# Kernel optimization log

Measured on AMD Instinct MI355X. Metric: run time of the kernel, lower is better.

The kernel has to match this reference:

```python
import jax, jax.numpy as jnp
import numpy as np

N_NODES = 10000
AVG_DEG = 16
N_EDGES = N_NODES * AVG_DEG
NODE_DIM, EDGE_DIM, LIN_DIM, HID, OUT, LAYERS = 9, 3, 32, 300, 2, 5


def _init(key, shape, fan_in):
    return jax.random.normal(key, shape, jnp.float32) * (1.0 / np.sqrt(fan_in))


def setup_inputs() -> dict:
    key = jax.random.key(0)
    ks = jax.random.split(key, 18)
    inp = {
        "x": jax.random.normal(ks[0], (N_NODES, NODE_DIM), jnp.float32),
        "edge_index": jax.random.randint(ks[1], (2, N_EDGES), 0, N_NODES, jnp.int32),
        "edge_attr": jax.random.normal(ks[2], (N_EDGES, EDGE_DIM), jnp.float32),
        "batch": jnp.zeros((N_NODES,), jnp.int32),
        # nn.Linear params (stored as [in, out] so fwd is x @ W + b)
        "node_w": _init(ks[3], (NODE_DIM, LIN_DIM), NODE_DIM),
        "node_b": jnp.zeros((LIN_DIM,), jnp.float32),
        "edge_w": _init(ks[4], (EDGE_DIM, LIN_DIM), EDGE_DIM),
        "edge_b": jnp.zeros((LIN_DIM,), jnp.float32),
        # GCNConv: lin (no bias) + separate additive bias (PyG convention)
        "gcn0_w": _init(ks[5], (LIN_DIM, HID), LIN_DIM),
        "gcn0_b": jnp.zeros((HID,), jnp.float32),
        "gcn_w": _init(ks[6], (LAYERS - 1, HID, HID), HID),
        "gcn_b": jnp.zeros((LAYERS - 1, HID), jnp.float32),
        "lin1_w": _init(ks[7], (HID, LIN_DIM), HID),
        "lin1_b": jnp.zeros((LIN_DIM,), jnp.float32),
        "lin2_w": _init(ks[8], (LIN_DIM, OUT), LIN_DIM),
        "lin2_b": jnp.zeros((OUT,), jnp.float32),
    }
    return inp


def reference(x, edge_index, edge_attr, batch,
              node_w, node_b, edge_w, edge_b,
              gcn0_w, gcn0_b, gcn_w, gcn_b,
              lin1_w, lin1_b, lin2_w, lin2_b):
    row, col = edge_index[0], edge_index[1]

    e = edge_attr @ edge_w + edge_b  # [E, LIN_DIM] edge embeddings

    # Faithful to the original bug: node embeddings get edge attrs scatter-added,
    # then the result is discarded by `attr = edge_attr`. Kept for fidelity (dead).
    node_h = x @ node_w + node_b
    node_h = node_h.at[row].add(e)  # unused downstream

    # GCN stack runs over the E-row edge-embedding matrix -> effective node count = E
    h = e
    n = h.shape[0]  # == N_EDGES

    # symmetric gcn_norm with self-loops (edge_weight = 1), computed once
    deg = jax.ops.segment_sum(jnp.ones((edge_index.shape[1],), h.dtype), col,
                              num_segments=n) + 1.0
    dinv = jax.lax.rsqrt(deg)
    norm = dinv[row] * dinv[col]  # per-edge normalization
    self_norm = (dinv * dinv)[:, None]  # self-loop term

    def gcn(h, w, b):
        hw = h @ w  # dense transform
        agg = jax.ops.segment_sum(hw[row] * norm[:, None], col, num_segments=n)
        return agg + self_norm * hw + b

    h = jax.nn.relu(gcn(h, gcn0_w, gcn0_b))

    def step(h, wb):
        w, b = wb
        return jax.nn.relu(gcn(h, w, b)), None

    h, _ = jax.lax.scan(step, h, (gcn_w, gcn_b))

    g = jnp.mean(h, axis=0, keepdims=True)  # [1, HID] graph readout
    g = jax.nn.relu(g @ lin1_w + lin1_b)
    pred = g @ lin2_w + lin2_b  # [1, OUT]; forward returns pre-softmax logits
    return pred
```

## Files before the change

### kernel.cpp

```cpp
#include <hip/hip_runtime.h>
#include <hip/hip_bf16.h>

#define N_NODES 10000
#define N_EDGES 160000
#define HID 300
#define HIDP 304
#define NPARTB (N_EDGES - N_NODES)
#define RB 64
#define KS 328

typedef __attribute__((ext_vector_type(8))) short short8;
typedef __attribute__((ext_vector_type(4))) float f32x4;

#define MFMA_B16(a, b, c) __builtin_amdgcn_mfma_f32_16x16x32_bf16(a, b, c, 0, 0, 0)

__device__ __forceinline__ short bf16r(float x) {
    unsigned u = __float_as_uint(x);
    return (short)((u + 0x7fffu + ((u >> 16) & 1u)) >> 16);
}

__device__ __forceinline__ float b2f(unsigned short u) {
    return __uint_as_float(((unsigned)u) << 16);
}

__device__ __forceinline__ void split1(float x, short& hi, short& lo) {
    short h = bf16r(x);
    float hf = __uint_as_float(((unsigned)(unsigned short)h) << 16);
    hi = h;
    lo = bf16r(x - hf);
}


__global__ void k_count(const int* __restrict__ col, int* __restrict__ cnt) {
    int e = blockIdx.x * 256 + threadIdx.x;
    if (e < N_EDGES) atomicAdd(&cnt[col[e]], 1);
}

__global__ void k_scan(const int* __restrict__ cnt, int* __restrict__ col_start,
                       int* __restrict__ cursor, float* __restrict__ dinv,
                       float* __restrict__ selfnorm) {
    __shared__ int wsum[4];
    int t = threadIdx.x;
    int lane = t & 63, w = t >> 6;
    int carry = 0;
    for (int base = 0; base < N_NODES; base += 256) {
        int i = base + t;
        int v = (i < N_NODES) ? cnt[i] : 0;
        int s = v;
#pragma unroll
        for (int d = 1; d < 64; d <<= 1) {
            int n = __shfl_up(s, d, 64);
            if (lane >= d) s += n;
        }
        if (lane == 63) wsum[w] = s;
        __syncthreads();
        int woff = 0;
#pragma unroll
        for (int k = 0; k < 4; ++k)
            if (k < w) woff += wsum[k];
        int total = wsum[0] + wsum[1] + wsum[2] + wsum[3];
        if (i < N_NODES) {
            int excl = carry + woff + s - v;
            col_start[i] = excl;
            cursor[i] = excl;
            float dd = (float)v + 1.0f;
            dinv[i] = rsqrtf(dd);
            selfnorm[i] = 1.0f / dd;
        }
        carry += total;
        __syncthreads();
    }
    if (t == 0) col_start[N_NODES] = carry;
}

__global__ void k_fill(const int* __restrict__ row, const int* __restrict__ col,
                       int* __restrict__ cursor, const float* __restrict__ dinv,
                       int2* __restrict__ edge_pack) {
    int e = blockIdx.x * 256 + threadIdx.x;
    if (e < N_EDGES) {
        int c = col[e], r = row[e];
        int p = atomicAdd(&cursor[c], 1);
        edge_pack[p] = make_int2(r, __float_as_int(dinv[r] * dinv[c]));
    }
}

__global__ void k_wt(const float* __restrict__ g0w, const float* __restrict__ gw,
                     short* __restrict__ wt0, short* __restrict__ wtl) {
    int idx = blockIdx.x * 256 + threadIdx.x;
    if (idx < 1216) {
        int n16 = idx & 15, q = (idx >> 4) & 3, nt = idx >> 6;
        int n = nt * 16 + n16;
        short* hd = wt0 + (size_t)(nt * 8 + q) * 128 + n16 * 8;
        short* ld = wt0 + (size_t)(nt * 8 + 4 + q) * 128 + n16 * 8;
#pragma unroll
        for (int j = 0; j < 8; ++j) {
            int k = q * 8 + j;
            float f = (n < HID) ? g0w[k * HID + n] : 0.0f;
            short hi, lo;
            split1(f, hi, lo);
            hd[j] = hi;
            ld[j] = lo;
        }
    } else if (idx < 1216 + 48640) {
        int i = idx - 1216;
        int n16 = i & 15; i >>= 4;
        int q = i & 3; i >>= 2;
        int nt = i % 19; i /= 19;
        int chunk = i % 10;
        int l = i / 10;
        int n = nt * 16 + n16;
        int cnt_idx = chunk * 19 + nt;
        short* base = wtl + (size_t)l * 194560;
        short* hd = base + (size_t)(cnt_idx * 8 + q) * 128 + n16 * 8;
        short* ld = base + (size_t)(cnt_idx * 8 + 4 + q) * 128 + n16 * 8;
#pragma unroll
        for (int j = 0; j < 8; ++j) {
            int k = chunk * 32 + q * 8 + j;
            float f = (k < HID && n < HID) ? gw[((size_t)l * HID + k) * HID + n] : 0.0f;
            short hi, lo;
            split1(f, hi, lo);
            hd[j] = hi;
            ld[j] = lo;
        }
    }
}


template <int NTC>
__device__ __forceinline__ void kloop(const short* __restrict__ wp, int nch,
                                      const short* Hh,
                                      int nt0, int quad, int l16,
                                      f32x4 (&acc)[4][3]) {
#pragma unroll
    for (int mt = 0; mt < 4; ++mt)
#pragma unroll
        for (int i = 0; i < NTC; ++i)
#pragma unroll
            for (int r = 0; r < 4; ++r) acc[mt][i][r] = 0.0f;
#pragma unroll 1
    for (int c = 0; c < nch; ++c) {
        short8 ah[4];
#pragma unroll
        for (int mt = 0; mt < 4; ++mt)
            ah[mt] = *(const short8*)&Hh[(mt * 16 + l16) * KS + c * 32 + quad * 8];
        const short* cb = wp + (size_t)(c * 19 + nt0) * 1024 + quad * 128 + l16 * 8;
        short8 bb[NTC];
#pragma unroll
        for (int i = 0; i < NTC; ++i) bb[i] = *(const short8*)(cb + (size_t)i * 1024);
#pragma unroll
        for (int mt = 0; mt < 4; ++mt)
#pragma unroll
            for (int i = 0; i < NTC; ++i)
                acc[mt][i] = MFMA_B16(ah[mt], bb[i], acc[mt][i]);
#pragma unroll
        for (int i = 0; i < NTC; ++i) bb[i] = *(const short8*)(cb + (size_t)i * 1024 + 512);
#pragma unroll
        for (int mt = 0; mt < 4; ++mt)
#pragma unroll
            for (int i = 0; i < NTC; ++i)
                acc[mt][i] = MFMA_B16(ah[mt], bb[i], acc[mt][i]);
    }
}

template <int NTC>
__device__ __forceinline__ void gcn_epilogue(const float* __restrict__ bias,
                                             int nt0, int quad, int l16,
                                             f32x4 (&acc)[4][3], short* Hh) {
#pragma unroll
    for (int i = 0; i < NTC; ++i) {
        int c = (nt0 + i) * 16 + l16;
        float b = (c < HID) ? bias[c] : 0.0f;
#pragma unroll
        for (int mt = 0; mt < 4; ++mt)
#pragma unroll
            for (int r = 0; r < 4; ++r) {
                float v = fmaxf(acc[mt][i][r] + b, 0.0f);
                Hh[(mt * 16 + quad * 4 + r) * KS + c] = bf16r(v);
            }
    }
}

template <int NTC>
__device__ __forceinline__ void gcn_final(const float* __restrict__ bias,
                                          int nt0, int quad, int l16,
                                          int valid, int slot,
                                          f32x4 (&acc)[4][3],
                                          float* __restrict__ g_part) {
#pragma unroll
    for (int i = 0; i < NTC; ++i) {
        int c = (nt0 + i) * 16 + l16;
        float b = (c < HID) ? bias[c] : 0.0f;
        float s = 0.0f;
#pragma unroll
        for (int mt = 0; mt < 4; ++mt)
#pragma unroll
            for (int r = 0; r < 4; ++r) {
                int rr = mt * 16 + quad * 4 + r;
                float v = fmaxf(acc[mt][i][r] + b, 0.0f);
                if (rr < valid) s += v;
            }
        s += __shfl_xor(s, 16, 64);
        s += __shfl_xor(s, 32, 64);
        if (quad == 0 && c < HID)
            atomicAdd(&g_part[slot * HIDP + c], s);
    }
}

__global__ __launch_bounds__(512, 4) void k_partB_mfma(
    const float* __restrict__ edge_attr,
    const float* __restrict__ edge_w,
    const float* __restrict__ edge_b,
    const short* __restrict__ wt0,
    const short* __restrict__ wtl,
    const float* __restrict__ b0,
    const float* __restrict__ gb,
    float* __restrict__ g_part) {
    __shared__ short Hh[RB * KS];
    int t = threadIdx.x;
    int lane = t & 63, w = t >> 6;
    int l16 = lane & 15, quad = lane >> 4;
    int base = N_NODES + blockIdx.x * RB;
    int nt0 = (w < 3) ? w * 3 : 9 + (w - 3) * 2;
    int valid = N_EDGES - base;

    {
        int r = t >> 3, c4 = (t & 7) * 4;
        int gr = base + r;
        float a0 = 0.f, a1 = 0.f, a2 = 0.f;
        if (gr < N_EDGES) {
            const float* ar = edge_attr + (size_t)gr * 3;
            a0 = ar[0]; a1 = ar[1]; a2 = ar[2];
        }
#pragma unroll
        for (int j = 0; j < 4; ++j) {
            int cc = c4 + j;
            float v = 0.0f;
            if (gr < N_EDGES) {
                v = edge_b[cc];
                v = fmaf(a0, edge_w[cc], v);
                v = fmaf(a1, edge_w[32 + cc], v);
                v = fmaf(a2, edge_w[64 + cc], v);
            }
            Hh[r * KS + cc] = bf16r(v);
        }
    }
    for (int i = t; i < RB * 24; i += 512) {
        int r = i / 24, k = 304 + i % 24;
        Hh[r * KS + k] = 0;
    }
    __syncthreads();

    f32x4 acc[4][3];
    if (w < 3) kloop<3>(wt0, 1, Hh, nt0, quad, l16, acc);
    else       kloop<2>(wt0, 1, Hh, nt0, quad, l16, acc);
    __syncthreads();
    if (w < 3) gcn_epilogue<3>(b0, nt0, quad, l16, acc, Hh);
    else       gcn_epilogue<2>(b0, nt0, quad, l16, acc, Hh);
    __syncthreads();

    for (int l = 0; l < 4; ++l) {
        const short* wp = wtl + (size_t)l * 194560;
        const float* bias = gb + l * HID;
        if (w < 3) kloop<3>(wp, 10, Hh, nt0, quad, l16, acc);
        else       kloop<2>(wp, 10, Hh, nt0, quad, l16, acc);
        __syncthreads();
        if (l < 3) {
            if (w < 3) gcn_epilogue<3>(bias, nt0, quad, l16, acc, Hh);
            else       gcn_epilogue<2>(bias, nt0, quad, l16, acc, Hh);
            __syncthreads();
        } else {
            int slot = (blockIdx.x + w) & 63;
            if (w < 3) gcn_final<3>(bias, nt0, quad, l16, valid, slot, acc, g_part);
            else       gcn_final<2>(bias, nt0, quad, l16, valid, slot, acc, g_part);
        }
    }
}

template <int NTC>
__device__ __forceinline__ void gemm_out(int base, int nt0, int quad, int l16,
                                         f32x4 (&acc)[4][3],
                                         unsigned short* __restrict__ HW) {
#pragma unroll
    for (int i = 0; i < NTC; ++i) {
        int c = (nt0 + i) * 16 + l16;
#pragma unroll
        for (int mt = 0; mt < 4; ++mt)
#pragma unroll
            for (int r = 0; r < 4; ++r) {
                int gm = base + mt * 16 + quad * 4 + r;
                if (gm < N_NODES)
                    HW[(size_t)gm * HIDP + c] = (unsigned short)bf16r(acc[mt][i][r]);
            }
    }
}

template <bool L0>
__global__ __launch_bounds__(512, 4) void k_gemmA(
    const unsigned short* __restrict__ A,
    const float* __restrict__ edge_attr,
    const float* __restrict__ edge_w,
    const float* __restrict__ edge_b,
    const short* __restrict__ wt,
    unsigned short* __restrict__ HW) {
    __shared__ short Hh[RB * KS];
    int t = threadIdx.x;
    int lane = t & 63, w = t >> 6;
    int l16 = lane & 15, quad = lane >> 4;
    int base = blockIdx.x * RB;
    int nt0 = (w < 3) ? w * 3 : 9 + (w - 3) * 2;

    if (L0) {
        int r = t >> 3, c4 = (t & 7) * 4;
        int gr = base + r;
        float a0 = 0.f, a1 = 0.f, a2 = 0.f;
        if (gr < N_NODES) {
            const float* ar = edge_attr + (size_t)gr * 3;
            a0 = ar[0]; a1 = ar[1]; a2 = ar[2];
        }
#pragma unroll
        for (int j = 0; j < 4; ++j) {
            int cc = c4 + j;
            float v = 0.0f;
            if (gr < N_NODES) {
                v = edge_b[cc];
                v = fmaf(a0, edge_w[cc], v);
                v = fmaf(a1, edge_w[32 + cc], v);
                v = fmaf(a2, edge_w[64 + cc], v);
            }
            Hh[r * KS + cc] = bf16r(v);
        }
    } else {
        for (int idx = t; idx < RB * 76; idx += 512) {
            int r = idx / 76, c4 = (idx % 76) * 4;
            int gr = base + r;
            ushort4 v = make_ushort4(0, 0, 0, 0);
            if (gr < N_NODES) v = *(const ushort4*)(A + (size_t)gr * HIDP + c4);
            short* d = &Hh[r * KS + c4];
            d[0] = (short)v.x; d[1] = (short)v.y; d[2] = (short)v.z; d[3] = (short)v.w;
        }
        for (int i = t; i < RB * 24; i += 512) {
            int r = i / 24, k = 304 + i % 24;
            Hh[r * KS + k] = 0;
        }
    }
    __syncthreads();

    f32x4 acc[4][3];
    if (L0) {
        if (w < 3) kloop<3>(wt, 1, Hh, nt0, quad, l16, acc);
        else       kloop<2>(wt, 1, Hh, nt0, quad, l16, acc);
    } else {
        if (w < 3) kloop<3>(wt, 10, Hh, nt0, quad, l16, acc);
        else       kloop<2>(wt, 10, Hh, nt0, quad, l16, acc);
    }
    if (w < 3) gemm_out<3>(base, nt0, quad, l16, acc, HW);
    else       gemm_out<2>(base, nt0, quad, l16, acc, HW);
}

__global__ __launch_bounds__(256) void k_aggA(
    const unsigned short* __restrict__ hw, const int* __restrict__ col_start,
    const int2* __restrict__ edge_pack, const float* __restrict__ selfnorm,
    const float* __restrict__ bias, unsigned short* __restrict__ out) {
    int wid = (blockIdx.x * 256 + threadIdx.x) >> 6;
    int lane = threadIdx.x & 63;
    int c = __builtin_amdgcn_readfirstlane(wid);
    if (c >= N_NODES) return;
    int beg = col_start[c], end = col_start[c + 1];
    float v[5] = {0.0f, 0.0f, 0.0f, 0.0f, 0.0f};
    int i = beg;
    for (; i + 4 <= end; i += 4) {
        int2 e0 = edge_pack[i], e1 = edge_pack[i + 1];
        int2 e2 = edge_pack[i + 2], e3 = edge_pack[i + 3];
        const unsigned short* h0 = hw + (size_t)e0.x * HIDP;
        const unsigned short* h1 = hw + (size_t)e1.x * HIDP;
        const unsigned short* h2 = hw + (size_t)e2.x * HIDP;
        const unsigned short* h3 = hw + (size_t)e3.x * HIDP;
        float n0 = __int_as_float(e0.y), n1 = __int_as_float(e1.y);
        float n2 = __int_as_float(e2.y), n3 = __int_as_float(e3.y);
#pragma unroll
        for (int j = 0; j < 5; ++j) {
            int col = lane + 64 * j;
            if (col < HIDP) {
                float s = v[j];
                s = fmaf(n0, b2f(h0[col]), s);
                s = fmaf(n1, b2f(h1[col]), s);
                s = fmaf(n2, b2f(h2[col]), s);
                s = fmaf(n3, b2f(h3[col]), s);
                v[j] = s;
            }
        }
    }
    for (; i < end; ++i) {
        int2 e0 = edge_pack[i];
        const unsigned short* h0 = hw + (size_t)e0.x * HIDP;
        float n0 = __int_as_float(e0.y);
#pragma unroll
        for (int j = 0; j < 5; ++j) {
            int col = lane + 64 * j;
            if (col < HIDP) v[j] = fmaf(n0, b2f(h0[col]), v[j]);
        }
    }
    float sn = selfnorm[c];
    const unsigned short* sp = hw + (size_t)c * HIDP;
#pragma unroll
    for (int j = 0; j < 5; ++j) {
        int col = lane + 64 * j;
        if (col < HIDP) {
            float h = v[j] + sn * b2f(sp[col]) + ((col < HID) ? bias[col] : 0.0f);
            out[(size_t)c * HIDP + col] = (unsigned short)bf16r(fmaxf(h, 0.0f));
        }
    }
}

__global__ void k_colsum(const unsigned short* __restrict__ h,
                         const float* __restrict__ g_part,
                         float* __restrict__ g_sum) {
    int b = blockIdx.x, t = threadIdx.x;
    if (b < 157) {
        int r0 = b * 64;
        float s0 = 0.0f, s1 = 0.0f;
        for (int r = 0; r < 64; ++r) {
            int gr = r0 + r;
            if (gr < N_NODES) {
                s0 += b2f(h[(size_t)gr * HIDP + t]);
                if (t < HIDP - 256) s1 += b2f(h[(size_t)gr * HIDP + 256 + t]);
            }
        }
        if (t < HID) atomicAdd(&g_sum[t], s0);
        if (t < HIDP - 256 && 256 + t < HID) atomicAdd(&g_sum[256 + t], s1);
    } else {
        int cc = (b - 157) * 256 + t;
        if (cc < HID) {
            float s = 0.0f;
            for (int g = 0; g < 64; ++g) s += g_part[g * HIDP + cc];
            atomicAdd(&g_sum[cc], s);
        }
    }
}

__global__ void k_head(const float* __restrict__ g_sum,
                       const float* __restrict__ lin1_w, const float* __restrict__ lin1_b,
                       const float* __restrict__ lin2_w, const float* __restrict__ lin2_b,
                       float* __restrict__ out) {
    __shared__ float g2[32];
    int t = threadIdx.x;
    const float inv = 1.0f / (float)N_EDGES;
    if (t < 32) {
        float a = lin1_b[t];
        for (int d = 0; d < HID; ++d) a = fmaf(g_sum[d] * inv, lin1_w[d * 32 + t], a);
        g2[t] = fmaxf(a, 0.0f);
    }
    __syncthreads();
    if (t < 2) {
        float p = lin2_b[t];
        for (int j = 0; j < 32; ++j) p = fmaf(g2[j], lin2_w[j * 2 + t], p);
        out[t] = p;
    }
}


extern "C" void kernel_launch(void* const* d_in, const int* in_sizes, int n_in,
                              void* d_out, int out_size, void* d_ws, size_t ws_size,
                              hipStream_t stream) {
    (void)in_sizes; (void)n_in; (void)out_size; (void)ws_size;
    const int* edge_index = (const int*)d_in[1];
    const float* edge_attr = (const float*)d_in[2];
    const float* edge_w = (const float*)d_in[6];
    const float* edge_b = (const float*)d_in[7];
    const float* gcn0_w = (const float*)d_in[8];
    const float* gcn0_b = (const float*)d_in[9];
    const float* gcn_w = (const float*)d_in[10];
    const float* gcn_b = (const float*)d_in[11];
    const float* lin1_w = (const float*)d_in[12];
    const float* lin1_b = (const float*)d_in[13];
    const float* lin2_w = (const float*)d_in[14];
    const float* lin2_b = (const float*)d_in[15];

    char* ws = (char*)d_ws;
    size_t off = 0;
    auto alloc = [&](size_t bytes) {
        void* p = ws + off;
        off = (off + bytes + 255) & ~(size_t)255;
        return p;
    };
    unsigned short* hA = (unsigned short*)alloc((size_t)N_NODES * HIDP * 2);
    unsigned short* hB = (unsigned short*)alloc((size_t)N_NODES * HIDP * 2);
    unsigned short* hw = (unsigned short*)alloc((size_t)N_NODES * HIDP * 2);
    int2* edge_pack = (int2*)alloc((size_t)N_EDGES * 8);
    int* cnt = (int*)alloc((size_t)N_NODES * 4);
    int* col_start = (int*)alloc((size_t)(N_NODES + 1) * 4);
    int* cursor = (int*)alloc((size_t)N_NODES * 4);
    float* dinv = (float*)alloc((size_t)N_NODES * 4);
    float* selfnorm = (float*)alloc((size_t)N_NODES * 4);
    float* g_sum = (float*)alloc((size_t)HIDP * 4);
    short* wt0 = (short*)alloc((size_t)38912);
    short* wtl = (short*)alloc((size_t)4 * 389120);
    float* g_part = (float*)alloc((size_t)64 * HIDP * 4);

    const int* row = edge_index;
    const int* col = edge_index + N_EDGES;

    hipMemsetAsync(cnt, 0, N_NODES * 4, stream);
    hipMemsetAsync(g_sum, 0, HIDP * 4, stream);
    hipMemsetAsync(g_part, 0, 64 * HIDP * 4, stream);

    k_wt<<<(1216 + 48640 + 255) / 256, 256, 0, stream>>>(gcn0_w, gcn_w, wt0, wtl);
    k_count<<<(N_EDGES + 255) / 256, 256, 0, stream>>>(col, cnt);
    k_scan<<<1, 256, 0, stream>>>(cnt, col_start, cursor, dinv, selfnorm);
    k_fill<<<(N_EDGES + 255) / 256, 256, 0, stream>>>(row, col, cursor, dinv, edge_pack);

    k_partB_mfma<<<(NPARTB + RB - 1) / RB, 512, 0, stream>>>(
        edge_attr, edge_w, edge_b, wt0, wtl, gcn0_b, gcn_b, g_part);

    const int gA_blocks = (N_NODES + RB - 1) / RB;
    const int aggA_blocks = (N_NODES + 3) / 4;
    k_gemmA<true><<<gA_blocks, 512, 0, stream>>>(nullptr, edge_attr, edge_w, edge_b, wt0, hw);
    k_aggA<<<aggA_blocks, 256, 0, stream>>>(hw, col_start, edge_pack, selfnorm, gcn0_b, hA);
    unsigned short* curr = hA;
    unsigned short* next = hB;
    for (int l = 1; l < 5; ++l) {
        k_gemmA<false><<<gA_blocks, 512, 0, stream>>>(curr, edge_attr, edge_w, edge_b,
                                                      wtl + (size_t)(l - 1) * 194560, hw);
        k_aggA<<<aggA_blocks, 256, 0, stream>>>(hw, col_start, edge_pack, selfnorm,
                                                gcn_b + (l - 1) * HID, next);
        unsigned short* tmp = curr; curr = next; next = tmp;
    }
    k_colsum<<<159, 256, 0, stream>>>(curr, g_part, g_sum);
    k_head<<<1, 64, 0, stream>>>(g_sum, lin1_w, lin1_b, lin2_w, lin2_b, (float*)d_out);
}
```

Measured before the change: 545.6 us.

## Fuse GCN stages into a mega-kernel and fused aggregate+GEMM kernels

The separate part-B, layer-0 GEMM and CSR-fill kernels become one heterogeneous mega-kernel dispatched by block index, and the count step is folded into weight preparation. Each layer's aggregation is fused with the next layer's GEMM, and the final aggregation is fused with the column-sum readout. Row tile size drops from 64 to 48 so 150000 part-B rows divide evenly, which removes bounds checks and allows higher occupancy. The aim is fewer launches and fewer intermediate HBM round trips, at the cost of less MFMA reuse per block and possibly imbalanced work across block types.

```diff
diff --git a/kernel.cpp b/kernel.cpp
--- a/kernel.cpp
+++ b/kernel.cpp
@@ -6,8 +6,12 @@
 #define HID 300
 #define HIDP 304
 #define NPARTB (N_EDGES - N_NODES)
-#define RB 64
+#define RB 48
 #define KS 328
+#define PARTB_BLOCKS 3125
+#define GEMMA_BLOCKS 209
+#define FILL_BLOCKS 313
+#define MEGA_BLOCKS (PARTB_BLOCKS + GEMMA_BLOCKS + FILL_BLOCKS)
 
 typedef __attribute__((ext_vector_type(8))) short short8;
 typedef __attribute__((ext_vector_type(4))) float f32x4;
@@ -30,63 +34,11 @@
     lo = bf16r(x - hf);
 }
 
-
-__global__ void k_count(const int* __restrict__ col, int* __restrict__ cnt) {
-    int e = blockIdx.x * 256 + threadIdx.x;
-    if (e < N_EDGES) atomicAdd(&cnt[col[e]], 1);
-}
-
-__global__ void k_scan(const int* __restrict__ cnt, int* __restrict__ col_start,
-                       int* __restrict__ cursor, float* __restrict__ dinv,
-                       float* __restrict__ selfnorm) {
-    __shared__ int wsum[4];
-    int t = threadIdx.x;
-    int lane = t & 63, w = t >> 6;
-    int carry = 0;
-    for (int base = 0; base < N_NODES; base += 256) {
-        int i = base + t;
-        int v = (i < N_NODES) ? cnt[i] : 0;
-        int s = v;
-#pragma unroll
-        for (int d = 1; d < 64; d <<= 1) {
-            int n = __shfl_up(s, d, 64);
-            if (lane >= d) s += n;
-        }
-        if (lane == 63) wsum[w] = s;
-        __syncthreads();
-        int woff = 0;
-#pragma unroll
-        for (int k = 0; k < 4; ++k)
-            if (k < w) woff += wsum[k];
-        int total = wsum[0] + wsum[1] + wsum[2] + wsum[3];
-        if (i < N_NODES) {
-            int excl = carry + woff + s - v;
-            col_start[i] = excl;
-            cursor[i] = excl;
-            float dd = (float)v + 1.0f;
-            dinv[i] = rsqrtf(dd);
-            selfnorm[i] = 1.0f / dd;
-        }
-        carry += total;
-        __syncthreads();
-    }
-    if (t == 0) col_start[N_NODES] = carry;
-}
-
-__global__ void k_fill(const int* __restrict__ row, const int* __restrict__ col,
-                       int* __restrict__ cursor, const float* __restrict__ dinv,
-                       int2* __restrict__ edge_pack) {
-    int e = blockIdx.x * 256 + threadIdx.x;
-    if (e < N_EDGES) {
-        int c = col[e], r = row[e];
-        int p = atomicAdd(&cursor[c], 1);
-        edge_pack[p] = make_int2(r, __float_as_int(dinv[r] * dinv[c]));
-    }
-}
-
-__global__ void k_wt(const float* __restrict__ g0w, const float* __restrict__ gw,
-                     short* __restrict__ wt0, short* __restrict__ wtl) {
+__global__ void k_prep(const float* __restrict__ g0w, const float* __restrict__ gw,
+                       short* __restrict__ wt0, short* __restrict__ wtl,
+                       const int* __restrict__ col, int* __restrict__ cnt) {
     int idx = blockIdx.x * 256 + threadIdx.x;
+    if (idx < N_EDGES) atomicAdd(&cnt[col[idx]], 1);
     if (idx < 1216) {
         int n16 = idx & 15, q = (idx >> 4) & 3, nt = idx >> 6;
         int n = nt * 16 + n16;
@@ -125,37 +77,73 @@
     }
 }
 
+__global__ void k_scan(const int* __restrict__ cnt, int* __restrict__ col_start,
+                       int* __restrict__ cursor, float* __restrict__ dinv,
+                       float* __restrict__ selfnorm) {
+    __shared__ int wsum[4];
+    int t = threadIdx.x;
+    int lane = t & 63, w = t >> 6;
+    int carry = 0;
+    for (int base = 0; base < N_NODES; base += 256) {
+        int i = base + t;
+        int v = (i < N_NODES) ? cnt[i] : 0;
+        int s = v;
+#pragma unroll
+        for (int d = 1; d < 64; d <<= 1) {
+            int n = __shfl_up(s, d, 64);
+            if (lane >= d) s += n;
+        }
+        if (lane == 63) wsum[w] = s;
+        __syncthreads();
+        int woff = 0;
+#pragma unroll
+        for (int k = 0; k < 4; ++k)
+            if (k < w) woff += wsum[k];
+        int total = wsum[0] + wsum[1] + wsum[2] + wsum[3];
+        if (i < N_NODES) {
+            int excl = carry + woff + s - v;
+            col_start[i] = excl;
+            cursor[i] = excl;
+            float dd = (float)v + 1.0f;
+            dinv[i] = rsqrtf(dd);
+            selfnorm[i] = 1.0f / dd;
+        }
+        carry += total;
+        __syncthreads();
+    }
+    if (t == 0) col_start[N_NODES] = carry;
+}
 
 template <int NTC>
 __device__ __forceinline__ void kloop(const short* __restrict__ wp, int nch,
                                       const short* Hh,
                                       int nt0, int quad, int l16,
-                                      f32x4 (&acc)[4][3]) {
-#pragma unroll
-    for (int mt = 0; mt < 4; ++mt)
+                                      f32x4 (&acc)[3][3]) {
+#pragma unroll
+    for (int mt = 0; mt < 3; ++mt)
 #pragma unroll
         for (int i = 0; i < NTC; ++i)
 #pragma unroll
             for (int r = 0; r < 4; ++r) acc[mt][i][r] = 0.0f;
 #pragma unroll 1
     for (int c = 0; c < nch; ++c) {
-        short8 ah[4];
-#pragma unroll
-        for (int mt = 0; mt < 4; ++mt)
+        const short* cb = wp + (size_t)(c * 19 + nt0) * 1024 + quad * 128 + l16 * 8;
+        short8 ah[3];
+#pragma unroll
+        for (int mt = 0; mt < 3; ++mt)
             ah[mt] = *(const short8*)&Hh[(mt * 16 + l16) * KS + c * 32 + quad * 8];
-        const short* cb = wp + (size_t)(c * 19 + nt0) * 1024 + quad * 128 + l16 * 8;
         short8 bb[NTC];
 #pragma unroll
         for (int i = 0; i < NTC; ++i) bb[i] = *(const short8*)(cb + (size_t)i * 1024);
 #pragma unroll
-        for (int mt = 0; mt < 4; ++mt)
+        for (int mt = 0; mt < 3; ++mt)
 #pragma unroll
             for (int i = 0; i < NTC; ++i)
                 acc[mt][i] = MFMA_B16(ah[mt], bb[i], acc[mt][i]);
 #pragma unroll
         for (int i = 0; i < NTC; ++i) bb[i] = *(const short8*)(cb + (size_t)i * 1024 + 512);
 #pragma unroll
-        for (int mt = 0; mt < 4; ++mt)
+        for (int mt = 0; mt < 3; ++mt)
 #pragma unroll
             for (int i = 0; i < NTC; ++i)
                 acc[mt][i] = MFMA_B16(ah[mt], bb[i], acc[mt][i]);
@@ -165,13 +153,13 @@
 template <int NTC>
 __device__ __forceinline__ void gcn_epilogue(const float* __restrict__ bias,
                                              int nt0, int quad, int l16,
-                                             f32x4 (&acc)[4][3], short* Hh) {
+                                             f32x4 (&acc)[3][3], short* Hh) {
 #pragma unroll
     for (int i = 0; i < NTC; ++i) {
         int c = (nt0 + i) * 16 + l16;
         float b = (c < HID) ? bias[c] : 0.0f;
 #pragma unroll
-        for (int mt = 0; mt < 4; ++mt)
+        for (int mt = 0; mt < 3; ++mt)
 #pragma unroll
             for (int r = 0; r < 4; ++r) {
                 float v = fmaxf(acc[mt][i][r] + b, 0.0f);
@@ -182,9 +170,8 @@
 
 template <int NTC>
 __device__ __forceinline__ void gcn_final(const float* __restrict__ bias,
-                                          int nt0, int quad, int l16,
-                                          int valid, int slot,
-                                          f32x4 (&acc)[4][3],
+                                          int nt0, int quad, int l16, int slot,
+                                          f32x4 (&acc)[3][3],
                                           float* __restrict__ g_part) {
 #pragma unroll
     for (int i = 0; i < NTC; ++i) {
@@ -192,13 +179,9 @@
         float b = (c < HID) ? bias[c] : 0.0f;
         float s = 0.0f;
 #pragma unroll
-        for (int mt = 0; mt < 4; ++mt)
-#pragma unroll
-            for (int r = 0; r < 4; ++r) {
-                int rr = mt * 16 + quad * 4 + r;
-                float v = fmaxf(acc[mt][i][r] + b, 0.0f);
-                if (rr < valid) s += v;
-            }
+        for (int mt = 0; mt < 3; ++mt)
+#pragma unroll
+            for (int r = 0; r < 4; ++r) s += fmaxf(acc[mt][i][r] + b, 0.0f);
         s += __shfl_xor(s, 16, 64);
         s += __shfl_xor(s, 32, 64);
         if (quad == 0 && c < HID)
@@ -206,102 +189,185 @@
     }
 }
 
-__global__ __launch_bounds__(512, 4) void k_partB_mfma(
+template <int NTC>
+__device__ __forceinline__ void gemm_out(int base, int nt0, int quad, int l16,
+                                         f32x4 (&acc)[3][3],
+                                         unsigned short* __restrict__ HW) {
+#pragma unroll
+    for (int i = 0; i < NTC; ++i) {
+        int c = (nt0 + i) * 16 + l16;
+#pragma unroll
+        for (int mt = 0; mt < 3; ++mt)
+#pragma unroll
+            for (int r = 0; r < 4; ++r) {
+                int gm = base + mt * 16 + quad * 4 + r;
+                if (gm < N_NODES)
+                    HW[(size_t)gm * HIDP + c] = (unsigned short)bf16r(acc[mt][i][r]);
+            }
+    }
+}
+
+__global__ __launch_bounds__(512, 6) void k_mega(
     const float* __restrict__ edge_attr,
     const float* __restrict__ edge_w,
     const float* __restrict__ edge_b,
     const short* __restrict__ wt0,
     const short* __restrict__ wtl,
-    const float* __restrict__ b0,
-    const float* __restrict__ gb,
-    float* __restrict__ g_part) {
+    const float* __restrict__ gcn0_b,
+    const float* __restrict__ gcn_b,
+    float* __restrict__ g_part,
+    unsigned short* __restrict__ hw0,
+    const int* __restrict__ row,
+    const int* __restrict__ col,
+    int* __restrict__ cursor,
+    const float* __restrict__ dinv,
+    int2* __restrict__ edge_pack) {
     __shared__ short Hh[RB * KS];
-    int t = threadIdx.x;
+    int bid = blockIdx.x, t = threadIdx.x;
     int lane = t & 63, w = t >> 6;
     int l16 = lane & 15, quad = lane >> 4;
-    int base = N_NODES + blockIdx.x * RB;
     int nt0 = (w < 3) ? w * 3 : 9 + (w - 3) * 2;
-    int valid = N_EDGES - base;
-
-    {
-        int r = t >> 3, c4 = (t & 7) * 4;
-        int gr = base + r;
-        float a0 = 0.f, a1 = 0.f, a2 = 0.f;
-        if (gr < N_EDGES) {
-            const float* ar = edge_attr + (size_t)gr * 3;
-            a0 = ar[0]; a1 = ar[1]; a2 = ar[2];
-        }
-#pragma unroll
-        for (int j = 0; j < 4; ++j) {
-            int cc = c4 + j;
-            float v = 0.0f;
-            if (gr < N_EDGES) {
-                v = edge_b[cc];
+
+    if (bid < PARTB_BLOCKS) {
+        int base = N_NODES + bid * RB;
+        if (t < 384) {
+            int r = t >> 3, c4 = (t & 7) * 4;
+            const float* ar = edge_attr + (size_t)(base + r) * 3;
+            float a0 = ar[0], a1 = ar[1], a2 = ar[2];
+#pragma unroll
+            for (int j = 0; j < 4; ++j) {
+                int cc = c4 + j;
+                float v = edge_b[cc];
                 v = fmaf(a0, edge_w[cc], v);
                 v = fmaf(a1, edge_w[32 + cc], v);
                 v = fmaf(a2, edge_w[64 + cc], v);
-            }
-            Hh[r * KS + cc] = bf16r(v);
-        }
-    }
-    for (int i = t; i < RB * 24; i += 512) {
-        int r = i / 24, k = 304 + i % 24;
-        Hh[r * KS + k] = 0;
-    }
-    __syncthreads();
-
-    f32x4 acc[4][3];
-    if (w < 3) kloop<3>(wt0, 1, Hh, nt0, quad, l16, acc);
-    else       kloop<2>(wt0, 1, Hh, nt0, quad, l16, acc);
-    __syncthreads();
-    if (w < 3) gcn_epilogue<3>(b0, nt0, quad, l16, acc, Hh);
-    else       gcn_epilogue<2>(b0, nt0, quad, l16, acc, Hh);
-    __syncthreads();
-
-    for (int l = 0; l < 4; ++l) {
-        const short* wp = wtl + (size_t)l * 194560;
-        const float* bias = gb + l * HID;
-        if (w < 3) kloop<3>(wp, 10, Hh, nt0, quad, l16, acc);
-        else       kloop<2>(wp, 10, Hh, nt0, quad, l16, acc);
+                Hh[r * KS + cc] = bf16r(v);
+            }
+        }
+        for (int i = t; i < RB * 24; i += 512) {
+            int r = i / 24, k = 304 + i % 24;
+            Hh[r * KS + k] = 0;
+        }
         __syncthreads();
-        if (l < 3) {
-            if (w < 3) gcn_epilogue<3>(bias, nt0, quad, l16, acc, Hh);
-            else       gcn_epilogue<2>(bias, nt0, quad, l16, acc, Hh);
+
+        f32x4 acc[3][3];
+        if (w < 3) kloop<3>(wt0, 1, Hh, nt0, quad, l16, acc);
+        else       kloop<2>(wt0, 1, Hh, nt0, quad, l16, acc);
+        __syncthreads();
+        if (w < 3) gcn_epilogue<3>(gcn0_b, nt0, quad, l16, acc, Hh);
+        else       gcn_epilogue<2>(gcn0_b, nt0, quad, l16, acc, Hh);
+        __syncthreads();
+
+        for (int l = 0; l < 4; ++l) {
+            const short* wp = wtl + (size_t)l * 194560;
+            const float* bias = gcn_b + l * HID;
+            if (w < 3) kloop<3>(wp, 10, Hh, nt0, quad, l16, acc);
+            else       kloop<2>(wp, 10, Hh, nt0, quad, l16, acc);
             __syncthreads();
-        } else {
-            int slot = (blockIdx.x + w) & 63;
-            if (w < 3) gcn_final<3>(bias, nt0, quad, l16, valid, slot, acc, g_part);
-            else       gcn_final<2>(bias, nt0, quad, l16, valid, slot, acc, g_part);
-        }
-    }
-}
-
-template <int NTC>
-__device__ __forceinline__ void gemm_out(int base, int nt0, int quad, int l16,
-                                         f32x4 (&acc)[4][3],
-                                         unsigned short* __restrict__ HW) {
-#pragma unroll
-    for (int i = 0; i < NTC; ++i) {
-        int c = (nt0 + i) * 16 + l16;
-#pragma unroll
-        for (int mt = 0; mt < 4; ++mt)
-#pragma unroll
-            for (int r = 0; r < 4; ++r) {
-                int gm = base + mt * 16 + quad * 4 + r;
-                if (gm < N_NODES)
-                    HW[(size_t)gm * HIDP + c] = (unsigned short)bf16r(acc[mt][i][r]);
-            }
-    }
-}
-
-template <bool L0>
-__global__ __launch_bounds__(512, 4) void k_gemmA(
-    const unsigned short* __restrict__ A,
-    const float* __restrict__ edge_attr,
-    const float* __restrict__ edge_w,
-    const float* __restrict__ edge_b,
+            if (l < 3) {
+                if (w < 3) gcn_epilogue<3>(bias, nt0, quad, l16, acc, Hh);
+                else       gcn_epilogue<2>(bias, nt0, quad, l16, acc, Hh);
+                __syncthreads();
+            } else {
+                int slot = (bid + w) & 63;
+                if (w < 3) gcn_final<3>(bias, nt0, quad, l16, slot, acc, g_part);
+                else       gcn_final<2>(bias, nt0, quad, l16, slot, acc, g_part);
+            }
+        }
+    } else if (bid < PARTB_BLOCKS + GEMMA_BLOCKS) {
+        int base = (bid - PARTB_BLOCKS) * RB;
+        if (t < 384) {
+            int r = t >> 3, c4 = (t & 7) * 4;
+            int gr = base + r;
+            float a0 = 0.f, a1 = 0.f, a2 = 0.f;
+            if (gr < N_NODES) {
+                const float* ar = edge_attr + (size_t)gr * 3;
+                a0 = ar[0]; a1 = ar[1]; a2 = ar[2];
+            }
+#pragma unroll
+            for (int j = 0; j < 4; ++j) {
+                int cc = c4 + j;
+                float v = 0.0f;
+                if (gr < N_NODES) {
+                    v = edge_b[cc];
+                    v = fmaf(a0, edge_w[cc], v);
+                    v = fmaf(a1, edge_w[32 + cc], v);
+                    v = fmaf(a2, edge_w[64 + cc], v);
+                }
+                Hh[r * KS + cc] = bf16r(v);
+            }
+        }
+        for (int i = t; i < RB * 24; i += 512) {
+            int r = i / 24, k = 304 + i % 24;
+            Hh[r * KS + k] = 0;
+        }
+        __syncthreads();
+        f32x4 acc[3][3];
+        if (w < 3) kloop<3>(wt0, 1, Hh, nt0, quad, l16, acc);
+        else       kloop<2>(wt0, 1, Hh, nt0, quad, l16, acc);
+        if (w < 3) gemm_out<3>(base, nt0, quad, l16, acc, hw0);
+        else       gemm_out<2>(base, nt0, quad, l16, acc, hw0);
+    } else {
+        int e = (bid - PARTB_BLOCKS - GEMMA_BLOCKS) * 512 + t;
+        if (e < N_EDGES) {
+            int c = col[e], r = row[e];
+            int p = atomicAdd(&cursor[c], 1);
+            edge_pack[p] = make_int2(r, __float_as_int(dinv[r] * dinv[c]));
+        }
+    }
+}
+
+__device__ __forceinline__ void agg_row(int c, int lane,
+                                        const unsigned short* __restrict__ hw_in,
+                                        const int* __restrict__ col_start,
+                                        const int2* __restrict__ edge_pack,
+                                        float (&v)[5]) {
+#pragma unroll
+    for (int jj = 0; jj < 5; ++jj) v[jj] = 0.0f;
+    int beg = col_start[c], end = col_start[c + 1];
+    int i = beg;
+    for (; i + 4 <= end; i += 4) {
+        int2 e0 = edge_pack[i], e1 = edge_pack[i + 1];
+        int2 e2 = edge_pack[i + 2], e3 = edge_pack[i + 3];
+        const unsigned short* h0 = hw_in + (size_t)e0.x * HIDP;
+        const unsigned short* h1 = hw_in + (size_t)e1.x * HIDP;
+        const unsigned short* h2 = hw_in + (size_t)e2.x * HIDP;
+        const unsigned short* h3 = hw_in + (size_t)e3.x * HIDP;
+        float n0 = __int_as_float(e0.y), n1 = __int_as_float(e1.y);
+        float n2 = __int_as_float(e2.y), n3 = __int_as_float(e3.y);
+#pragma unroll
+        for (int jj = 0; jj < 5; ++jj) {
+            int cc = lane + 64 * jj;
+            if (cc < HIDP) {
+                float s = v[jj];
+                s = fmaf(n0, b2f(h0[cc]), s);
+                s = fmaf(n1, b2f(h1[cc]), s);
+                s = fmaf(n2, b2f(h2[cc]), s);
+                s = fmaf(n3, b2f(h3[cc]), s);
+                v[jj] = s;
+            }
+        }
+    }
+    for (; i < end; ++i) {
+        int2 e0 = edge_pack[i];
+        const unsigned short* h0 = hw_in + (size_t)e0.x * HIDP;
+        float n0 = __int_as_float(e0.y);
+#pragma unroll
+        for (int jj = 0; jj < 5; ++jj) {
+            int cc = lane + 64 * jj;
+            if (cc < HIDP) v[jj] = fmaf(n0, b2f(h0[cc]), v[jj]);
+        }
+    }
+}
+
+__global__ __launch_bounds__(512, 6) void k_fuse(
+    const unsigned short* __restrict__ hw_in,
+    const int* __restrict__ col_start,
+    const int2* __restrict__ edge_pack,
+    const float* __restrict__ selfnorm,
+    const float* __restrict__ bias,
     const short* __restrict__ wt,
-    unsigned short* __restrict__ HW) {
+    unsigned short* __restrict__ hw_out) {
     __shared__ short Hh[RB * KS];
     int t = threadIdx.x;
     int lane = t & 63, w = t >> 6;
@@ -309,145 +375,110 @@
     int base = blockIdx.x * RB;
     int nt0 = (w < 3) ? w * 3 : 9 + (w - 3) * 2;
 
-    if (L0) {
-        int r = t >> 3, c4 = (t & 7) * 4;
-        int gr = base + r;
-        float a0 = 0.f, a1 = 0.f, a2 = 0.f;
-        if (gr < N_NODES) {
-            const float* ar = edge_attr + (size_t)gr * 3;
-            a0 = ar[0]; a1 = ar[1]; a2 = ar[2];
-        }
-#pragma unroll
-        for (int j = 0; j < 4; ++j) {
-            int cc = c4 + j;
-            float v = 0.0f;
-            if (gr < N_NODES) {
-                v = edge_b[cc];
-                v = fmaf(a0, edge_w[cc], v);
-                v = fmaf(a1, edge_w[32 + cc], v);
-                v = fmaf(a2, edge_w[64 + cc], v);
-            }
-            Hh[r * KS + cc] = bf16r(v);
-        }
-    } else {
-        for (int idx = t; idx < RB * 76; idx += 512) {
-            int r = idx / 76, c4 = (idx % 76) * 4;
-            int gr = base + r;
-            ushort4 v = make_ushort4(0, 0, 0, 0);
-            if (gr < N_NODES) v = *(const ushort4*)(A + (size_t)gr * HIDP + c4);
-            short* d = &Hh[r * KS + c4];
-            d[0] = (short)v.x; d[1] = (short)v.y; d[2] = (short)v.z; d[3] = (short)v.w;
-        }
-        for (int i = t; i < RB * 24; i += 512) {
-            int r = i / 24, k = 304 + i % 24;
-            Hh[r * KS + k] = 0;
-        }
+#pragma unroll 1
+    for (int j = 0; j < 6; ++j) {
+        int r = w * 6 + j;
+        int c = base + r;
+        if (c < N_NODES) {
+            float v[5];
+            agg_row(c, lane, hw_in, col_start, edge_pack, v);
+            float sn = selfnorm[c];
+            const unsigned short* sp = hw_in + (size_t)c * HIDP;
+#pragma unroll
+            for (int jj = 0; jj < 5; ++jj) {
+                int cc = lane + 64 * jj;
+                if (cc < HIDP) {
+                    float h = v[jj] + sn * b2f(sp[cc]) + ((cc < HID) ? bias[cc] : 0.0f);
+                    Hh[r * KS + cc] = bf16r(fmaxf(h, 0.0f));
+                }
+            }
+        } else {
+#pragma unroll
+            for (int jj = 0; jj < 5; ++jj) {
+                int cc = lane + 64 * jj;
+                if (cc < HIDP) Hh[r * KS + cc] = 0;
+            }
+        }
+    }
+    for (int i = t; i < RB * 24; i += 512) {
+        int r = i / 24, k = 304 + i % 24;
+        Hh[r * KS + k] = 0;
     }
     __syncthreads();
 
-    f32x4 acc[4][3];
-    if (L0) {
-        if (w < 3) kloop<3>(wt, 1, Hh, nt0, quad, l16, acc);
-        else       kloop<2>(wt, 1, Hh, nt0, quad, l16, acc);
-    } else {
-        if (w < 3) kloop<3>(wt, 10, Hh, nt0, quad, l16, acc);
-        else       kloop<2>(wt, 10, Hh, nt0, quad, l16, acc);
-    }
-    if (w < 3) gemm_out<3>(base, nt0, quad, l16, acc, HW);
-    else       gemm_out<2>(base, nt0, quad, l16, acc, HW);
-}
-
-__global__ __launch_bounds__(256) void k_aggA(
-    const unsigned short* __restrict__ hw, const int* __restrict__ col_start,
-    const int2* __restrict__ edge_pack, const float* __restrict__ selfnorm,
-    const float* __restrict__ bias, unsigned short* __restrict__ out) {
-    int wid = (blockIdx.x * 256 + threadIdx.x) >> 6;
-    int lane = threadIdx.x & 63;
-    int c = __builtin_amdgcn_readfirstlane(wid);
-    if (c >= N_NODES) return;
-    int beg = col_start[c], end = col_start[c + 1];
-    float v[5] = {0.0f, 0.0f, 0.0f, 0.0f, 0.0f};
-    int i = beg;
-    for (; i + 4 <= end; i += 4) {
-        int2 e0 = edge_pack[i], e1 = edge_pack[i + 1];
-        int2 e2 = edge_pack[i + 2], e3 = edge_pack[i + 3];
-        const unsigned short* h0 = hw + (size_t)e0.x * HIDP;
-        const unsigned short* h1 = hw + (size_t)e1.x * HIDP;
-        const unsigned short* h2 = hw + (size_t)e2.x * HIDP;
-        const unsigned short* h3 = hw + (size_t)e3.x * HIDP;
-        float n0 = __int_as_float(e0.y), n1 = __int_as_float(e1.y);
-        float n2 = __int_as_float(e2.y), n3 = __int_as_float(e3.y);
-#pragma unroll
-        for (int j = 0; j < 5; ++j) {
-            int col = lane + 64 * j;
-            if (col < HIDP) {
-                float s = v[j];
-                s = fmaf(n0, b2f(h0[col]), s);
-                s = fmaf(n1, b2f(h1[col]), s);
-                s = fmaf(n2, b2f(h2[col]), s);
-                s = fmaf(n3, b2f(h3[col]), s);
-                v[j] = s;
-            }
-        }
-    }
-    for (; i < end; ++i) {
-        int2 e0 = edge_pack[i];
-        const unsigned short* h0 = hw + (size_t)e0.x * HIDP;
-        float n0 = __int_as_float(e0.y);
-#pragma unroll
-        for (int j = 0; j < 5; ++j) {
-            int col = lane + 64 * j;
-            if (col < HIDP) v[j] = fmaf(n0, b2f(h0[col]), v[j]);
-        }
-    }
-    float sn = selfnorm[c];
-    const unsigned short* sp = hw + (size_t)c * HIDP;
-#pragma unroll
-    for (int j = 0; j < 5; ++j) {
-        int col = lane + 64 * j;
-        if (col < HIDP) {
-            float h = v[j] + sn * b2f(sp[col]) + ((col < HID) ? bias[col] : 0.0f);
-            out[(size_t)c * HIDP + col] = (unsigned short)bf16r(fmaxf(h, 0.0f));
-        }
-    }
-}
-
-__global__ void k_colsum(const unsigned short* __restrict__ h,
-                         const float* __restrict__ g_part,
-                         float* __restrict__ g_sum) {
-    int b = blockIdx.x, t = threadIdx.x;
-    if (b < 157) {
-        int r0 = b * 64;
-        float s0 = 0.0f, s1 = 0.0f;
-        for (int r = 0; r < 64; ++r) {
-            int gr = r0 + r;
-            if (gr < N_NODES) {
-                s0 += b2f(h[(size_t)gr * HIDP + t]);
-                if (t < HIDP - 256) s1 += b2f(h[(size_t)gr * HIDP + 256 + t]);
-            }
-        }
-        if (t < HID) atomicAdd(&g_sum[t], s0);
-        if (t < HIDP - 256 && 256 + t < HID) atomicAdd(&g_sum[256 + t], s1);
-    } else {
-        int cc = (b - 157) * 256 + t;
-        if (cc < HID) {
-            float s = 0.0f;
-            for (int g = 0; g < 64; ++g) s += g_part[g * HIDP + cc];
-            atomicAdd(&g_sum[cc], s);
+    f32x4 acc[3][3];
+    if (w < 3) kloop<3>(wt, 10, Hh, nt0, quad, l16, acc);
+    else       kloop<2>(wt, 10, Hh, nt0, quad, l16, acc);
+    if (w < 3) gemm_out<3>(base, nt0, quad, l16, acc, hw_out);
+    else       gemm_out<2>(base, nt0, quad, l16, acc, hw_out);
+}
+
+__global__ __launch_bounds__(512) void k_last(
+    const unsigned short* __restrict__ hw_in,
+    const int* __restrict__ col_start,
+    const int2* __restrict__ edge_pack,
+    const float* __restrict__ selfnorm,
+    const float* __restrict__ bias,
+    float* __restrict__ g_sum) {
+    __shared__ float red[8 * 320];
+    int t = threadIdx.x;
+    int lane = t & 63, w = t >> 6;
+    int base = blockIdx.x * RB;
+
+    float s[5] = {0.0f, 0.0f, 0.0f, 0.0f, 0.0f};
+#pragma unroll 1
+    for (int j = 0; j < 6; ++j) {
+        int c = base + w * 6 + j;
+        if (c < N_NODES) {
+            float v[5];
+            agg_row(c, lane, hw_in, col_start, edge_pack, v);
+            float sn = selfnorm[c];
+            const unsigned short* sp = hw_in + (size_t)c * HIDP;
+#pragma unroll
+            for (int jj = 0; jj < 5; ++jj) {
+                int cc = lane + 64 * jj;
+                if (cc < HID) {
+                    float h = v[jj] + sn * b2f(sp[cc]) + bias[cc];
+                    s[jj] += fmaxf(h, 0.0f);
+                }
+            }
+        }
+    }
+#pragma unroll
+    for (int jj = 0; jj < 5; ++jj) red[w * 320 + lane + 64 * jj] = s[jj];
+    __syncthreads();
+    if (w == 0) {
+#pragma unroll
+        for (int jj = 0; jj < 5; ++jj) {
+            int cc = lane + 64 * jj;
+            if (cc < HID) {
+                float tot = 0.0f;
+#pragma unroll
+                for (int g = 0; g < 8; ++g) tot += red[g * 320 + cc];
+                atomicAdd(&g_sum[cc], tot);
+            }
         }
     }
 }
 
 __global__ void k_head(const float* __restrict__ g_sum,
+                       const float* __restrict__ g_part,
                        const float* __restrict__ lin1_w, const float* __restrict__ lin1_b,
                        const float* __restrict__ lin2_w, const float* __restrict__ lin2_b,
                        float* __restrict__ out) {
+    __shared__ float gm[HID];
     __shared__ float g2[32];
     int t = threadIdx.x;
     const float inv = 1.0f / (float)N_EDGES;
+    for (int c = t; c < HID; c += 256) {
+        float s = g_sum[c];
+        for (int g = 0; g < 64; ++g) s += g_part[g * HIDP + c];
+        gm[c] = s * inv;
+    }
+    __syncthreads();
     if (t < 32) {
         float a = lin1_b[t];
-        for (int d = 0; d < HID; ++d) a = fmaf(g_sum[d] * inv, lin1_w[d * 32 + t], a);
+        for (int d = 0; d < HID; ++d) a = fmaf(gm[d], lin1_w[d * 32 + t], a);
         g2[t] = fmaxf(a, 0.0f);
     }
     __syncthreads();
@@ -483,9 +514,8 @@
         off = (off + bytes + 255) & ~(size_t)255;
         return p;
     };
-    unsigned short* hA = (unsigned short*)alloc((size_t)N_NODES * HIDP * 2);
-    unsigned short* hB = (unsigned short*)alloc((size_t)N_NODES * HIDP * 2);
-    unsigned short* hw = (unsigned short*)alloc((size_t)N_NODES * HIDP * 2);
+    unsigned short* hwA = (unsigned short*)alloc((size_t)N_NODES * HIDP * 2);
+    unsigned short* hwB = (unsigned short*)alloc((size_t)N_NODES * HIDP * 2);
     int2* edge_pack = (int2*)alloc((size_t)N_EDGES * 8);
     int* cnt = (int*)alloc((size_t)N_NODES * 4);
     int* col_start = (int*)alloc((size_t)(N_NODES + 1) * 4);
@@ -504,27 +534,23 @@
     hipMemsetAsync(g_sum, 0, HIDP * 4, stream);
     hipMemsetAsync(g_part, 0, 64 * HIDP * 4, stream);
 
-    k_wt<<<(1216 + 48640 + 255) / 256, 256, 0, stream>>>(gcn0_w, gcn_w, wt0, wtl);
-    k_count<<<(N_EDGES + 255) / 256, 256, 0, stream>>>(col, cnt);
+    k_prep<<<(N_EDGES + 255) / 256, 256, 0, stream>>>(gcn0_w, gcn_w, wt0, wtl, col, cnt);
     k_scan<<<1, 256, 0, stream>>>(cnt, col_start, cursor, dinv, selfnorm);
-    k_fill<<<(N_EDGES + 255) / 256, 256, 0, stream>>>(row, col, cursor, dinv, edge_pack);
-
-    k_partB_mfma<<<(NPARTB + RB - 1) / RB, 512, 0, stream>>>(
-        edge_attr, edge_w, edge_b, wt0, wtl, gcn0_b, gcn_b, g_part);
-
-    const int gA_blocks = (N_NODES + RB - 1) / RB;
-    const int aggA_blocks = (N_NODES + 3) / 4;
-    k_gemmA<true><<<gA_blocks, 512, 0, stream>>>(nullptr, edge_attr, edge_w, edge_b, wt0, hw);
-    k_aggA<<<aggA_blocks, 256, 0, stream>>>(hw, col_start, edge_pack, selfnorm, gcn0_b, hA);
-    unsigned short* curr = hA;
-    unsigned short* next = hB;
-    for (int l = 1; l < 5; ++l) {
-        k_gemmA<false><<<gA_blocks, 512, 0, stream>>>(curr, edge_attr, edge_w, edge_b,
-                                                      wtl + (size_t)(l - 1) * 194560, hw);
-        k_aggA<<<aggA_blocks, 256, 0, stream>>>(hw, col_start, edge_pack, selfnorm,
-                                                gcn_b + (l - 1) * HID, next);
-        unsigned short* tmp = curr; curr = next; next = tmp;
-    }
-    k_colsum<<<159, 256, 0, stream>>>(curr, g_part, g_sum);
-    k_head<<<1, 64, 0, stream>>>(g_sum, lin1_w, lin1_b, lin2_w, lin2_b, (float*)d_out);
-}
+
+    k_mega<<<MEGA_BLOCKS, 512, 0, stream>>>(edge_attr, edge_w, edge_b, wt0, wtl,
+                                            gcn0_b, gcn_b, g_part, hwA,
+                                            row, col, cursor, dinv, edge_pack);
+
+    k_fuse<<<GEMMA_BLOCKS, 512, 0, stream>>>(hwA, col_start, edge_pack, selfnorm,
+                                             gcn0_b, wtl + (size_t)0 * 194560, hwB);
+    k_fuse<<<GEMMA_BLOCKS, 512, 0, stream>>>(hwB, col_start, edge_pack, selfnorm,
+                                             gcn_b + 0 * HID, wtl + (size_t)1 * 194560, hwA);
+    k_fuse<<<GEMMA_BLOCKS, 512, 0, stream>>>(hwA, col_start, edge_pack, selfnorm,
+                                             gcn_b + 1 * HID, wtl + (size_t)2 * 194560, hwB);
+    k_fuse<<<GEMMA_BLOCKS, 512, 0, stream>>>(hwB, col_start, edge_pack, selfnorm,
+                                             gcn_b + 2 * HID, wtl + (size_t)3 * 194560, hwA);
+    k_last<<<GEMMA_BLOCKS, 512, 0, stream>>>(hwA, col_start, edge_pack, selfnorm,
+                                             gcn_b + 3 * HID, g_sum);
+    k_head<<<1, 256, 0, stream>>>(g_sum, g_part, lin1_w, lin1_b, lin2_w, lin2_b,
+                                  (float*)d_out);
+}
```

New measurement: 637.2 us. 1.17x slower.
